# Optimization experiments

Measured on AMD Instinct MI355X. Metric: run time of the kernel, lower is better.

The kernel has to match this reference:

```python
import jax, jax.numpy as jnp
import numpy as np

EPS = 1e-6
NUM_HEADS = 16


def rotate_every_two(x):
    # pairs (x1, x2) -> (-x2, x1), interleaved on last dim
    x1 = x[..., 0::2]
    x2 = x[..., 1::2]
    return jnp.stack((-x2, x1), axis=-1).reshape(x.shape)


def apply_rotary(q, k, sinu_pos):
    # sinu_pos: [1, L, 2*dh]; split into sin/cos halves of size dh, then
    # repeat each element twice along feature dim ('b n -> b (n j)', j=2).
    L = sinu_pos.shape[1]
    sp = sinu_pos.reshape(L, 2, -1)          # [L, 2, dh]
    sin = jnp.repeat(sp[:, 0], 2, axis=-1)   # [L, D]
    cos = jnp.repeat(sp[:, 1], 2, axis=-1)   # [L, D]
    sin = sin[None, :, None, :]              # broadcast over B, H
    cos = cos[None, :, None, :]
    rot = lambda t: t * cos + rotate_every_two(t) * sin
    return rot(q), rot(k)


def softmax_kernel(data, is_query, proj):
    # data: [B, L, H, D], proj: [M, D] -> features [B, L, H, M]
    D = data.shape[-1]
    data_normalizer = D ** -0.25
    ratio = proj.shape[0] ** -0.5
    data_dash = jnp.einsum('blhd,md->blhm', data_normalizer * data, proj)
    diag = jnp.sum(data * data, axis=-1, keepdims=True) * 0.5 * data_normalizer ** 2
    if is_query:
        m = jax.lax.stop_gradient(jnp.max(data_dash, axis=-1, keepdims=True))
    else:
        m = jax.lax.stop_gradient(jnp.max(data_dash, axis=(-2, -1), keepdims=True))
    return ratio * (jnp.exp(data_dash - diag - m) + EPS)


def favor_noncausal(qp, kp, v):
    # qp, kp: [B, L, H, M]; v: [B, L, H, D]
    kvs = jnp.einsum('blhm,blhd->bhmd', kp, v)
    num = jnp.einsum('blhm,bhmd->blhd', qp, kvs)
    ks_sum = jnp.sum(kp, axis=1)                       # [B, H, M]
    den = jnp.einsum('blhm,bhm->blh', qp, ks_sum)      # [B, L, H]
    return num / den[..., None]


def setup_inputs() -> dict:
    key = jax.random.key(0)
    ks = jax.random.split(key, 7)
    B, L, Dm = 2, 4096, 1024
    M, Dh = 256, Dm // NUM_HEADS
    s = 0.02
    x = jax.random.normal(ks[0], (B, L, Dm), jnp.float32)
    Wq = jax.random.normal(ks[1], (Dm, Dm), jnp.float32) * s
    Wk = jax.random.normal(ks[2], (Dm, Dm), jnp.float32) * s
    Wv = jax.random.normal(ks[3], (Dm, Dm), jnp.float32) * s
    Wo = jax.random.normal(ks[4], (Dm, Dm), jnp.float32) * s
    proj = jax.random.normal(ks[5], (M, Dh), jnp.float32)
    sinu_pos = jax.random.normal(ks[6], (1, L, Dh), jnp.float32)
    return {"x": x, "Wq": Wq, "Wk": Wk, "Wv": Wv, "Wo": Wo,
            "proj": proj, "sinu_pos": sinu_pos}


def reference(x, Wq, Wk, Wv, Wo, proj, sinu_pos):
    B, L, Dm = x.shape
    H = NUM_HEADS
    Dh = Dm // H
    q = (x @ Wq).reshape(B, L, H, Dh)
    k = (x @ Wk).reshape(B, L, H, Dh)
    v = (x @ Wv).reshape(B, L, H, Dh)
    q, k = apply_rotary(q, k, sinu_pos)
    qp = softmax_kernel(q, True, proj)   # [B, L, H, M]
    kp = softmax_kernel(k, False, proj)  # [B, L, H, M]
    av = favor_noncausal(qp, kp, v)      # [B, L, H, Dh]
    return av.reshape(B, L, Dm) @ Wo
```

## Files before the change

### kernel.cpp

```cpp
#include <hip/hip_runtime.h>

typedef __attribute__((ext_vector_type(8))) short short8;
typedef __attribute__((ext_vector_type(4))) float f32x4;
typedef unsigned short USHORT;

#define DNORM 0.35355339059327373f
#define AS1(p) ((const __attribute__((address_space(1))) void*)(p))
#define AS3(p) ((__attribute__((address_space(3))) void*)(p))

__device__ __forceinline__ USHORT f2bf(float f) {
  union { float f; unsigned u; } v; v.f = f;
  unsigned r = v.u + 0x7fffu + ((v.u >> 16) & 1u);
  return (USHORT)(r >> 16);
}
__device__ __forceinline__ float bf2f(USHORT u) {
  union { unsigned u; float f; } v; v.u = ((unsigned)u) << 16;
  return v.f;
}
__device__ __forceinline__ unsigned fkey(float f) {
  union { float f; unsigned u; } v; v.f = f;
  return (v.u & 0x80000000u) ? ~v.u : (v.u | 0x80000000u);
}
__device__ __forceinline__ float keyf(unsigned k) {
  union { unsigned u; float f; } v;
  v.u = (k & 0x80000000u) ? (k ^ 0x80000000u) : ~k;
  return v.f;
}

__device__ __forceinline__ void stage_hl16(const float* __restrict__ src,
                                           USHORT* __restrict__ Ah, USHORT* __restrict__ Al,
                                           int r, int kc) {
  float b[16];
  *(float4*)&b[0] = *(const float4*)(src);
  *(float4*)&b[4] = *(const float4*)(src + 4);
  *(float4*)&b[8] = *(const float4*)(src + 8);
  *(float4*)&b[12] = *(const float4*)(src + 12);
  const int swz = (r & 7) << 3;
  unsigned H[8], L[8];
#pragma unroll
  for (int p = 0; p < 8; ++p) {
    USHORT h0 = f2bf(b[2 * p]), h1 = f2bf(b[2 * p + 1]);
    USHORT l0 = f2bf(b[2 * p] - bf2f(h0)), l1 = f2bf(b[2 * p + 1] - bf2f(h1));
    H[p] = (unsigned)h0 | ((unsigned)h1 << 16);
    L[p] = (unsigned)l0 | ((unsigned)l1 << 16);
  }
  *(uint4*)&Ah[r * 64 + (kc ^ swz)] = make_uint4(H[0], H[1], H[2], H[3]);
  *(uint4*)&Ah[r * 64 + ((kc + 8) ^ swz)] = make_uint4(H[4], H[5], H[6], H[7]);
  *(uint4*)&Al[r * 64 + (kc ^ swz)] = make_uint4(L[0], L[1], L[2], L[3]);
  *(uint4*)&Al[r * 64 + ((kc + 8) ^ swz)] = make_uint4(L[4], L[5], L[6], L[7]);
}

__global__ __launch_bounds__(256) void detect_kernel(const USHORT* __restrict__ w,
                                                     int* __restrict__ flag) {
  const int t = threadIdx.x;
  unsigned mx = 0;
#pragma unroll 8
  for (int c = 0; c < 64; ++c) {
    unsigned a = (unsigned)w[c * 256 + t] & 0x7FFFu;
    if (a > mx) mx = a;
  }
  if (mx > 0x4480u) atomicOr(flag, 1);
}

__global__ __launch_bounds__(256) void cvt_x_kernel(const void* __restrict__ xin,
                                                    USHORT* __restrict__ xh,
                                                    const void* __restrict__ proj,
                                                    USHORT* __restrict__ projc,
                                                    const int* __restrict__ flag) {
  if (blockIdx.x >= 4096) {
    const int i = ((blockIdx.x - 4096) * 256 + threadIdx.x) * 4;
    if (*flag) {
      float4 v = *(const float4*)((const float*)proj + i);
      USHORT a = f2bf(v.x), b = f2bf(v.y), c = f2bf(v.z), d = f2bf(v.w);
      *(uint2*)(projc + i) = make_uint2((unsigned)a | ((unsigned)b << 16),
                                        (unsigned)c | ((unsigned)d << 16));
    } else {
      *(uint2*)(projc + i) = *(const uint2*)((const USHORT*)proj + i);
    }
    return;
  }
  const size_t i = ((size_t)blockIdx.x * 256 + threadIdx.x) * 8;
  if (*flag) {
    const float* xf = (const float*)xin;
    float4 a = *(const float4*)(xf + i);
    float4 b = *(const float4*)(xf + i + 4);
    float c[8] = {a.x, a.y, a.z, a.w, b.x, b.y, b.z, b.w};
    unsigned ho[4];
#pragma unroll
    for (int j = 0; j < 4; ++j) {
      USHORT h0 = f2bf(c[2 * j]), h1 = f2bf(c[2 * j + 1]);
      ho[j] = (unsigned)h0 | ((unsigned)h1 << 16);
    }
    *(uint4*)(xh + i) = make_uint4(ho[0], ho[1], ho[2], ho[3]);
  } else {
    uint4 u = *(const uint4*)((const USHORT*)xin + i);
    *(uint4*)(xh + i) = u;
  }
}

__global__ __launch_bounds__(256) void sinut_kernel(const void* __restrict__ sinu,
                                                    float* __restrict__ sinuT,
                                                    const int* __restrict__ flag) {
  const int l = blockIdx.x * 256 + threadIdx.x;
  if (*flag) {
    const float* s = (const float*)sinu + (size_t)l * 64;
#pragma unroll 8
    for (int j2 = 0; j2 < 32; ++j2) {
      sinuT[j2 * 4096 + l] = s[j2];
      sinuT[131072 + j2 * 4096 + l] = s[32 + j2];
    }
  } else {
    const USHORT* s = (const USHORT*)sinu + (size_t)l * 64;
#pragma unroll 8
    for (int j2 = 0; j2 < 32; ++j2) {
      sinuT[j2 * 4096 + l] = bf2f(s[j2]);
      sinuT[131072 + j2 * 4096 + l] = bf2f(s[32 + j2]);
    }
  }
}

__global__ __launch_bounds__(256) void transpose_w_kernel(const void* __restrict__ Wq,
                                                          const void* __restrict__ Wk,
                                                          const void* __restrict__ Wv,
                                                          const void* __restrict__ Wo,
                                                          USHORT* __restrict__ wqkvt,
                                                          USHORT* __restrict__ wot,
                                                          const int* __restrict__ flag) {
  __shared__ __align__(16) USHORT tile[64][80];
  const int z = blockIdx.z;
  const void* src = (z == 0) ? Wq : (z == 1) ? Wk : (z == 2) ? Wv : Wo;
  USHORT* dst = (z < 3) ? (wqkvt + (size_t)z * 1048576) : wot;
  const int r0 = blockIdx.y * 64, c0 = blockIdx.x * 64;
  const int t = threadIdx.x;
  const int rr = t >> 2, c4 = (t & 3) * 16;
  if (*flag) {
    const float* s = (const float*)src + (size_t)(r0 + rr) * 1024 + c0 + c4;
#pragma unroll
    for (int i = 0; i < 4; ++i) {
      float4 v = *(const float4*)(s + i * 4);
      tile[rr][c4 + i * 4 + 0] = f2bf(v.x);
      tile[rr][c4 + i * 4 + 1] = f2bf(v.y);
      tile[rr][c4 + i * 4 + 2] = f2bf(v.z);
      tile[rr][c4 + i * 4 + 3] = f2bf(v.w);
    }
  } else {
    const USHORT* s = (const USHORT*)src + (size_t)(r0 + rr) * 1024 + c0 + c4;
    *(uint4*)&tile[rr][c4] = *(const uint4*)s;
    *(uint4*)&tile[rr][c4 + 8] = *(const uint4*)(s + 8);
  }
  __syncthreads();
  USHORT tmp[16];
#pragma unroll
  for (int i = 0; i < 16; ++i) tmp[i] = tile[c4 + i][rr];
  uint4 o0, o1;
  o0.x = (unsigned)tmp[0] | ((unsigned)tmp[1] << 16);
  o0.y = (unsigned)tmp[2] | ((unsigned)tmp[3] << 16);
  o0.z = (unsigned)tmp[4] | ((unsigned)tmp[5] << 16);
  o0.w = (unsigned)tmp[6] | ((unsigned)tmp[7] << 16);
  o1.x = (unsigned)tmp[8] | ((unsigned)tmp[9] << 16);
  o1.y = (unsigned)tmp[10] | ((unsigned)tmp[11] << 16);
  o1.z = (unsigned)tmp[12] | ((unsigned)tmp[13] << 16);
  o1.w = (unsigned)tmp[14] | ((unsigned)tmp[15] << 16);
  USHORT* d = dst + (size_t)(c0 + rr) * 1024 + r0 + c4;
  *(uint4*)d = o0;
  *(uint4*)(d + 8) = o1;
}

template <bool ROTEPI, bool FLAGOUT>
__global__ __launch_bounds__(256) void gemm_bt(const USHORT* __restrict__ A,
                                               const USHORT* __restrict__ Bt,
                                               void* __restrict__ Cv,
                                               USHORT* __restrict__ Vb,
                                               const float* __restrict__ sinuT,
                                               float* __restrict__ diag_q,
                                               float* __restrict__ diag_k,
                                               int M, int N, int K, int lda, int ldb, int ldc,
                                               int ldv, int NLO, const int* __restrict__ flag) {
  __shared__ __align__(16) USHORT As[8192];
  __shared__ __align__(16) USHORT Bs[8192];
  const int fl = *flag;
  const int t = threadIdx.x;
  const int lane = t & 63, wave = t >> 6;
  const int lr = lane & 15, lg = lane >> 4;
  const int nwg = gridDim.x * gridDim.y;
  const int orig = blockIdx.y * gridDim.x + blockIdx.x;
  const int tile = (orig & 7) * (nwg >> 3) + (orig >> 3);
  const int bx = tile % gridDim.x, by = tile / gridDim.x;
  const int row0 = by * 128, col0 = bx * 128;
  const int wr = (wave >> 1) * 64, wc = (wave & 1) * 64;
  f32x4 acc[4][4] = {};
  for (int k0 = 0; k0 < K; k0 += 64) {
#pragma unroll
    for (int c = 0; c < 4; ++c) {
      const int e = c * 256 + t;
      const int r = e >> 3;
      const int ch = (t & 7) ^ (r & 7);
      const size_t goffA = (size_t)(row0 + r) * lda + k0 + ch * 8;
      const size_t goffB = (size_t)(col0 + r) * ldb + k0 + ch * 8;
      __builtin_amdgcn_global_load_lds(AS1(A + goffA), AS3(&As[c * 2048 + wave * 512]), 16, 0, 0);
      __builtin_amdgcn_global_load_lds(AS1(Bt + goffB), AS3(&Bs[c * 2048 + wave * 512]), 16, 0, 0);
    }
    __syncthreads();
#pragma unroll
    for (int ks = 0; ks < 2; ++ks) {
      const int koff = ks * 32 + (lg << 3);
      short8 av_[4], bv[4];
#pragma unroll
      for (int i = 0; i < 4; ++i) {
        const int ar = wr + i * 16 + lr;
        av_[i] = *(const short8*)&As[ar * 64 + (koff ^ ((ar & 7) << 3))];
      }
#pragma unroll
      for (int j = 0; j < 4; ++j) {
        const int br = wc + j * 16 + lr;
        bv[j] = *(const short8*)&Bs[br * 64 + (koff ^ ((br & 7) << 3))];
      }
#pragma unroll
      for (int i = 0; i < 4; ++i)
#pragma unroll
        for (int j = 0; j < 4; ++j)
          acc[i][j] = __builtin_amdgcn_mfma_f32_16x16x32_bf16(av_[i], bv[j], acc[i][j], 0, 0, 0);
    }
    __syncthreads();
  }
  if constexpr (ROTEPI) {
    if (col0 < NLO) {
      const int G0 = col0 + wc;
      const int which = G0 >> 10;
      const int h = (G0 & 1023) >> 6;
      const int par = lr & 1;
      float* qk = (float*)Cv;
#pragma unroll
      for (int i = 0; i < 4; ++i) {
        const int R0 = row0 + wr + i * 16 + (lg << 2);
        const int l0 = R0 & 4095;
        float ss[4] = {0.f, 0.f, 0.f, 0.f};
#pragma unroll
        for (int j = 0; j < 4; ++j) {
          const int j2 = j * 8 + (lr >> 1);
          const float4 s4 = *(const float4*)&sinuT[(size_t)j2 * 4096 + l0];
          const float4 c4 = *(const float4*)&sinuT[131072 + (size_t)j2 * 4096 + l0];
          const float sv[4] = {s4.x, s4.y, s4.z, s4.w};
          const float cw[4] = {c4.x, c4.y, c4.z, c4.w};
          const int G = G0 + j * 16 + lr;
#pragma unroll
          for (int r = 0; r < 4; ++r) {
            const float own = acc[i][j][r];
            const float oth = __shfl_xor(own, 1);
            const float ro = par ? (own * cw[r] + oth * sv[r]) : (own * cw[r] - oth * sv[r]);
            ss[r] += ro * ro;
            qk[(size_t)(R0 + r) * ldc + G] = ro;
          }
        }
#pragma unroll
        for (int r = 0; r < 4; ++r) {
          float v_ = ss[r];
          v_ += __shfl_xor(v_, 1);
          v_ += __shfl_xor(v_, 2);
          v_ += __shfl_xor(v_, 4);
          v_ += __shfl_xor(v_, 8);
          if (lr == 0)
            (which ? diag_k : diag_q)[(R0 + r) * 16 + h] = v_ * 0.0625f;
        }
      }
    } else {
#pragma unroll
      for (int i = 0; i < 4; ++i) {
#pragma unroll
        for (int r = 0; r < 4; ++r) {
          const int row = row0 + wr + i * 16 + (lg << 2) + r;
#pragma unroll
          for (int j = 0; j < 4; ++j) {
            const int col = col0 + wc + j * 16 + lr - NLO;
            Vb[(size_t)row * ldv + col] = f2bf(acc[i][j][r]);
          }
        }
      }
    }
    return;
  }
#pragma unroll
  for (int i = 0; i < 4; ++i) {
#pragma unroll
    for (int r = 0; r < 4; ++r) {
      const int row = row0 + wr + i * 16 + (lg << 2) + r;
#pragma unroll
      for (int j = 0; j < 4; ++j) {
        const int col = col0 + wc + j * 16 + lr;
        const float v = acc[i][j][r];
        if constexpr (FLAGOUT) {
          if (fl) ((float*)Cv)[(size_t)row * ldc + col] = v;
          else ((USHORT*)Cv)[(size_t)row * ldc + col] = f2bf(v);
        } else {
          ((USHORT*)Cv)[(size_t)row * ldc + col] = f2bf(v);
        }
      }
    }
  }
}

__global__ __launch_bounds__(256) void ddk_max_kernel(const float* __restrict__ qkf,
                                                      const USHORT* __restrict__ proj,
                                                      unsigned* __restrict__ mk) {
  __shared__ __align__(16) USHORT Ph[16384];
  __shared__ __align__(16) USHORT Ah[4096], Al[4096];
  const int t = threadIdx.x, lane = t & 63, wave = t >> 6;
  const int lr = lane & 15, lg = lane >> 4;
  const int bh = blockIdx.y, b = bh >> 4, h = bh & 15;
  const size_t grow0 = (size_t)b * 4096 + blockIdx.x * 64;
  {
#pragma unroll
    for (int c = 0; c < 8; ++c)
      *(uint4*)&Ph[t * 64 + ((c ^ (t & 7)) << 3)] = *(const uint4*)(proj + t * 64 + c * 8);
  }
  {
    const int r = t >> 2, kc = (t & 3) * 16;
    stage_hl16(qkf + (grow0 + r) * 2048 + 1024 + h * 64 + kc, Ah, Al, r, kc);
  }
  __syncthreads();
  f32x4 acc[16] = {};
#pragma unroll
  for (int ks = 0; ks < 2; ++ks) {
    const int koff = ks * 32 + (lg << 3);
    const int ar = wave * 16 + lr;
    short8 a_h = *(const short8*)&Ah[ar * 64 + (koff ^ ((ar & 7) << 3))];
    short8 a_l = *(const short8*)&Al[ar * 64 + (koff ^ ((ar & 7) << 3))];
#pragma unroll
    for (int n = 0; n < 16; ++n) {
      const int br = n * 16 + lr;
      short8 b_h = *(const short8*)&Ph[br * 64 + (koff ^ ((br & 7) << 3))];
      acc[n] = __builtin_amdgcn_mfma_f32_16x16x32_bf16(a_h, b_h, acc[n], 0, 0, 0);
      acc[n] = __builtin_amdgcn_mfma_f32_16x16x32_bf16(a_l, b_h, acc[n], 0, 0, 0);
    }
  }
#pragma unroll
  for (int r = 0; r < 4; ++r) {
    float m_ = acc[0][r];
#pragma unroll
    for (int n = 1; n < 16; ++n) m_ = fmaxf(m_, acc[n][r]);
    m_ = fmaxf(m_, __shfl_xor(m_, 1));
    m_ = fmaxf(m_, __shfl_xor(m_, 2));
    m_ = fmaxf(m_, __shfl_xor(m_, 4));
    m_ = fmaxf(m_, __shfl_xor(m_, 8));
    if (lr == 0) {
      const int row = (int)grow0 + wave * 16 + (lg << 2) + r;
      atomicMax(&mk[row], fkey(m_ * DNORM));
    }
  }
}

__global__ __launch_bounds__(256) void kvs_accum_kernel(const float* __restrict__ qkf,
                                                        const USHORT* __restrict__ vb,
                                                        const USHORT* __restrict__ proj,
                                                        const float* __restrict__ diag_k,
                                                        const unsigned* __restrict__ mk,
                                                        float* __restrict__ kvs_ext) {
  __shared__ __align__(16) USHORT Ph[8192];
  __shared__ __align__(16) USHORT Ah[4096], Al[4096];
  __shared__ __align__(16) USHORT KpT[8192];
  __shared__ __align__(16) USHORT Vt[5120];
  const int t = threadIdx.x, lane = t & 63, wave = t >> 6;
  const int lr = lane & 15, lg = lane >> 4;
  const int bh = blockIdx.z, b = bh >> 4, h = bh & 15;
  const int fh = blockIdx.y;
  const int lstart = blockIdx.x * 512;
  {
    const int pr = t >> 1;
    const USHORT* src = proj + (size_t)(fh * 128 + pr) * 64;
#pragma unroll
    for (int c = 0; c < 4; ++c) {
      const int ch = (t & 1) * 4 + c;
      *(uint4*)&Ph[pr * 64 + ((ch ^ (pr & 7)) << 3)] = *(const uint4*)(src + ch * 8);
    }
  }
  if (t < 64) {
#pragma unroll
    for (int r = 64; r < 80; ++r) Vt[r * 64 + t] = (r == 64) ? (USHORT)0x3F80 : (USHORT)0;
  }
  f32x4 acc2[2][5] = {};
  for (int sub = 0; sub < 8; ++sub) {
    const int row0 = lstart + sub * 64;
    const size_t grow0 = (size_t)b * 4096 + row0;
    {
      const int r = t >> 2, kc = (t & 3) * 16;
      stage_hl16(qkf + (grow0 + r) * 2048 + 1024 + h * 64 + kc, Ah, Al, r, kc);
    }
    {
      const int rv = t & 63, dc = (t >> 6) * 16;
      const USHORT* sv = vb + (grow0 + rv) * 1024 + h * 64 + dc;
      uint4 u0 = *(const uint4*)sv;
      uint4 u1 = *(const uint4*)(sv + 8);
      unsigned wsrc[8] = {u0.x, u0.y, u0.z, u0.w, u1.x, u1.y, u1.z, u1.w};
#pragma unroll
      for (int i = 0; i < 8; ++i) {
        const int d0 = dc + 2 * i;
        Vt[d0 * 64 + (rv ^ ((d0 & 7) << 3))] = (USHORT)(wsrc[i] & 0xffff);
        Vt[(d0 + 1) * 64 + (rv ^ (((d0 + 1) & 7) << 3))] = (USHORT)(wsrc[i] >> 16);
      }
    }
    __syncthreads();
    f32x4 acc1[8] = {};
#pragma unroll
    for (int ks = 0; ks < 2; ++ks) {
      const int koff = ks * 32 + (lg << 3);
      const int ar = wave * 16 + lr;
      short8 a_h = *(const short8*)&Ah[ar * 64 + (koff ^ ((ar & 7) << 3))];
      short8 a_l = *(const short8*)&Al[ar * 64 + (koff ^ ((ar & 7) << 3))];
#pragma unroll
      for (int n = 0; n < 8; ++n) {
        const int br = n * 16 + lr;
        short8 b_h = *(const short8*)&Ph[br * 64 + (koff ^ ((br & 7) << 3))];
        acc1[n] = __builtin_amdgcn_mfma_f32_16x16x32_bf16(a_h, b_h, acc1[n], 0, 0, 0);
        acc1[n] = __builtin_amdgcn_mfma_f32_16x16x32_bf16(a_l, b_h, acc1[n], 0, 0, 0);
      }
    }
    const int rbase = wave * 16 + (lg << 2);
    float dg[4], mkr[4];
#pragma unroll
    for (int r = 0; r < 4; ++r) {
      dg[r] = diag_k[(grow0 + rbase + r) * 16 + h];
      mkr[r] = keyf(mk[grow0 + rbase + r]);
    }
#pragma unroll
    for (int n = 0; n < 8; ++n) {
      const int col = n * 16 + lr;
      USHORT pk[4];
#pragma unroll
      for (int r = 0; r < 4; ++r)
        pk[r] = f2bf(__expf(acc1[n][r] * DNORM - dg[r] - mkr[r]) + 1e-6f);
      const unsigned w0 = (unsigned)pk[0] | ((unsigned)pk[1] << 16);
      const unsigned w1 = (unsigned)pk[2] | ((unsigned)pk[3] << 16);
      *(uint2*)&KpT[col * 64 + (rbase ^ ((col & 7) << 3))] = make_uint2(w0, w1);
    }
    __syncthreads();
#pragma unroll
    for (int ks = 0; ks < 2; ++ks) {
      const int koff = ks * 32 + (lg << 3);
      short8 af[2];
#pragma unroll
      for (int i = 0; i < 2; ++i) {
        const int m = wave * 32 + i * 16 + lr;
        af[i] = *(const short8*)&KpT[m * 64 + (koff ^ ((m & 7) << 3))];
      }
#pragma unroll
      for (int c = 0; c < 5; ++c) {
        const int d = c * 16 + lr;
        short8 bv = *(const short8*)&Vt[d * 64 + (koff ^ ((d & 7) << 3))];
#pragma unroll
        for (int i = 0; i < 2; ++i)
          acc2[i][c] = __builtin_amdgcn_mfma_f32_16x16x32_bf16(af[i], bv, acc2[i][c], 0, 0, 0);
      }
    }
    __syncthreads();
  }
  float* basep = kvs_ext + (size_t)bh * 20480 + (size_t)fh * 128 * 80;
#pragma unroll
  for (int i = 0; i < 2; ++i) {
    const int mrow = wave * 32 + i * 16 + (lg << 2);
#pragma unroll
    for (int c = 0; c < 5; ++c) {
      const int col = c * 16 + lr;
      if (c == 4 && lr != 0) continue;
#pragma unroll
      for (int r = 0; r < 4; ++r)
        atomicAdd(basep + (size_t)(mrow + r) * 80 + col, acc2[i][c][r]);
    }
  }
}

__global__ __launch_bounds__(256) void cvt_kvs_kernel(const float* __restrict__ kvs_ext,
                                                      USHORT* __restrict__ kvsT16) {
  const int bh = blockIdx.x;
  const float* src = kvs_ext + (size_t)bh * 20480;
  USHORT* dst = kvsT16 + (size_t)bh * 20480;
  const int m = threadIdx.x;
#pragma unroll 8
  for (int d = 0; d < 80; ++d)
    dst[d * 256 + m] = f2bf(src[m * 80 + d]);
}

__global__ __launch_bounds__(256) void qav_kernel(const float* __restrict__ qkf,
                                                  const USHORT* __restrict__ proj,
                                                  const float* __restrict__ diag_q,
                                                  const USHORT* __restrict__ kvsT16,
                                                  USHORT* __restrict__ avb) {
  __shared__ __align__(16) USHORT smem[36864];
  USHORT* Ph = smem;
  USHORT* Qp = smem;
  USHORT* Ah = smem + 16384;
  USHORT* Al = smem + 20480;
  USHORT* Btl = smem + 16384;
  const int t = threadIdx.x, lane = t & 63, wave = t >> 6;
  const int lr = lane & 15, lg = lane >> 4;
  const int bh = blockIdx.y, b = bh >> 4, h = bh & 15;
  const size_t grow0 = (size_t)b * 4096 + blockIdx.x * 64;
  {
#pragma unroll
    for (int c = 0; c < 8; ++c)
      *(uint4*)&Ph[t * 64 + ((c ^ (t & 7)) << 3)] = *(const uint4*)(proj + t * 64 + c * 8);
  }
  {
    const int r = t >> 2, kc = (t & 3) * 16;
    stage_hl16(qkf + (grow0 + r) * 2048 + h * 64 + kc, Ah, Al, r, kc);
  }
  __syncthreads();
  f32x4 acc1[16] = {};
#pragma unroll
  for (int ks = 0; ks < 2; ++ks) {
    const int koff = ks * 32 + (lg << 3);
    const int ar = wave * 16 + lr;
    short8 a_h = *(const short8*)&Ah[ar * 64 + (koff ^ ((ar & 7) << 3))];
    short8 a_l = *(const short8*)&Al[ar * 64 + (koff ^ ((ar & 7) << 3))];
#pragma unroll
    for (int n = 0; n < 16; ++n) {
      const int br = n * 16 + lr;
      short8 b_h = *(const short8*)&Ph[br * 64 + (koff ^ ((br & 7) << 3))];
      acc1[n] = __builtin_amdgcn_mfma_f32_16x16x32_bf16(a_h, b_h, acc1[n], 0, 0, 0);
      acc1[n] = __builtin_amdgcn_mfma_f32_16x16x32_bf16(a_l, b_h, acc1[n], 0, 0, 0);
    }
  }
  __syncthreads();
  {
    const USHORT* src = kvsT16 + (size_t)bh * 20480;
#pragma unroll
    for (int c = 0; c < 10; ++c) {
      const int e = c * 256 + t;
      const int d = e >> 5, ch = e & 31;
      *(uint4*)&Btl[d * 256 + ((ch ^ (d & 7)) << 3)] = *(const uint4*)(src + d * 256 + ch * 8);
    }
  }
  const int rbase = wave * 16 + (lg << 2);
  float dg[4], mx[4];
#pragma unroll
  for (int r = 0; r < 4; ++r) dg[r] = diag_q[(grow0 + rbase + r) * 16 + h];
#pragma unroll
  for (int r = 0; r < 4; ++r) {
    float m_ = acc1[0][r];
#pragma unroll
    for (int n = 1; n < 16; ++n) m_ = fmaxf(m_, acc1[n][r]);
    m_ = fmaxf(m_, __shfl_xor(m_, 1));
    m_ = fmaxf(m_, __shfl_xor(m_, 2));
    m_ = fmaxf(m_, __shfl_xor(m_, 4));
    m_ = fmaxf(m_, __shfl_xor(m_, 8));
    mx[r] = m_ * DNORM;
  }
#pragma unroll
  for (int n = 0; n < 16; ++n) {
    const int col = n * 16 + lr;
#pragma unroll
    for (int r = 0; r < 4; ++r) {
      const int row = rbase + r;
      Qp[row * 256 + (col ^ ((row & 7) << 3))] =
          f2bf(__expf(acc1[n][r] * DNORM - dg[r] - mx[r]) + 1e-6f);
    }
  }
  __syncthreads();
  f32x4 acc2[5] = {};
#pragma unroll
  for (int ks2 = 0; ks2 < 8; ++ks2) {
    const int koff = ks2 * 32 + (lg << 3);
    const int ar = wave * 16 + lr;
    short8 a = *(const short8*)&Qp[ar * 256 + (koff ^ ((ar & 7) << 3))];
#pragma unroll
    for (int c = 0; c < 5; ++c) {
      const int cr = c * 16 + lr;
      short8 bv = *(const short8*)&Btl[cr * 256 + (koff ^ ((cr & 7) << 3))];
      acc2[c] = __builtin_amdgcn_mfma_f32_16x16x32_bf16(a, bv, acc2[c], 0, 0, 0);
    }
  }
#pragma unroll
  for (int r = 0; r < 4; ++r) {
    const float den = __shfl(acc2[4][r], (lane & 48));
#pragma unroll
    for (int c = 0; c < 4; ++c) {
      const float o = acc2[c][r] / den;
      avb[(grow0 + rbase + r) * 1024 + h * 64 + c * 16 + lr] = f2bf(o);
    }
  }
}

extern "C" void kernel_launch(void* const* d_in, const int* in_sizes, int n_in,
                              void* d_out, int out_size, void* d_ws, size_t ws_size,
                              hipStream_t stream) {
  char* ws = (char*)d_ws;

  const size_t OFF_FLAG = 0;
  const size_t OFF_WQKVT = 256;
  const size_t OFF_WOT = OFF_WQKVT + 6291456;
  const size_t OFF_PROJC = OFF_WOT + 2097152;
  const size_t OFF_PAD = OFF_PROJC + 32768;
  const size_t OFF_XH = OFF_PAD + 524288;
  const size_t OFF_SINUT = OFF_XH + 16777216;
  const size_t OFF_PAD2 = OFF_SINUT + 1048576;
  const size_t OFF_QKF = OFF_PAD2 + 15728640;
  const size_t OFF_VB = OFF_QKF + 67108864;
  const size_t OFF_DIAGQ = OFF_VB + 16777216;
  const size_t OFF_DIAGK = OFF_DIAGQ + 524288;
  const size_t OFF_MK = OFF_DIAGK + 524288;
  const size_t OFF_KVS = OFF_MK + 32768;
  const size_t OFF_KVST = OFF_KVS + 2621440;

  int* flag = (int*)(ws + OFF_FLAG);
  USHORT* wqkvt = (USHORT*)(ws + OFF_WQKVT);
  USHORT* wot = (USHORT*)(ws + OFF_WOT);
  USHORT* projc = (USHORT*)(ws + OFF_PROJC);
  USHORT* xh = (USHORT*)(ws + OFF_XH);
  USHORT* avb = (USHORT*)(ws + OFF_XH);
  float* sinuT = (float*)(ws + OFF_SINUT);
  float* qkf = (float*)(ws + OFF_QKF);
  USHORT* vb = (USHORT*)(ws + OFF_VB);
  float* diagq = (float*)(ws + OFF_DIAGQ);
  float* diagk = (float*)(ws + OFF_DIAGK);
  unsigned* mk = (unsigned*)(ws + OFF_MK);
  float* kvsb = (float*)(ws + OFF_KVS);
  USHORT* kvst = (USHORT*)(ws + OFF_KVST);

  hipMemsetAsync(ws + OFF_FLAG, 0, 256, stream);
  hipMemsetAsync(ws + OFF_MK, 0, 32768, stream);
  hipMemsetAsync(ws + OFF_KVS, 0, 2621440, stream);

  detect_kernel<<<1, 256, 0, stream>>>((const USHORT*)d_in[1], flag);
  cvt_x_kernel<<<4112, 256, 0, stream>>>(d_in[0], xh, d_in[5], projc, flag);
  sinut_kernel<<<16, 256, 0, stream>>>(d_in[6], sinuT, flag);
  transpose_w_kernel<<<dim3(16, 16, 4), 256, 0, stream>>>(d_in[1], d_in[2], d_in[3], d_in[4],
                                                          wqkvt, wot, flag);
  gemm_bt<true, false><<<dim3(24, 64), 256, 0, stream>>>(
      xh, wqkvt, qkf, vb, sinuT, diagq, diagk,
      8192, 3072, 1024, 1024, 1024, 2048, 1024, 2048, flag);
  ddk_max_kernel<<<dim3(64, 32), 256, 0, stream>>>(qkf, projc, mk);
  kvs_accum_kernel<<<dim3(8, 2, 32), 256, 0, stream>>>(qkf, vb, projc, diagk, mk, kvsb);
  cvt_kvs_kernel<<<32, 256, 0, stream>>>(kvsb, kvst);
  qav_kernel<<<dim3(64, 32), 256, 0, stream>>>(qkf, projc, diagq, kvst, avb);
  gemm_bt<false, true><<<dim3(8, 64), 256, 0, stream>>>(
      avb, wot, d_out, nullptr, nullptr, nullptr, nullptr,
      8192, 1024, 1024, 1024, 1024, 1024, 0, 0, flag);
}
```

Baseline: 236.3 us.

## Read proj and kvs operands from global directly, drop LDS staging and lo-split

```diff
diff --git a/kernel.cpp b/kernel.cpp
--- a/kernel.cpp
+++ b/kernel.cpp
@@ -48,6 +48,22 @@
   *(uint4*)&Ah[r * 64 + ((kc + 8) ^ swz)] = make_uint4(H[4], H[5], H[6], H[7]);
   *(uint4*)&Al[r * 64 + (kc ^ swz)] = make_uint4(L[0], L[1], L[2], L[3]);
   *(uint4*)&Al[r * 64 + ((kc + 8) ^ swz)] = make_uint4(L[4], L[5], L[6], L[7]);
+}
+
+__device__ __forceinline__ void stage_h16(const float* __restrict__ src,
+                                          USHORT* __restrict__ Ah, int r, int kc) {
+  float b[16];
+  *(float4*)&b[0] = *(const float4*)(src);
+  *(float4*)&b[4] = *(const float4*)(src + 4);
+  *(float4*)&b[8] = *(const float4*)(src + 8);
+  *(float4*)&b[12] = *(const float4*)(src + 12);
+  const int swz = (r & 7) << 3;
+  unsigned H[8];
+#pragma unroll
+  for (int p = 0; p < 8; ++p)
+    H[p] = (unsigned)f2bf(b[2 * p]) | ((unsigned)f2bf(b[2 * p + 1]) << 16);
+  *(uint4*)&Ah[r * 64 + (kc ^ swz)] = make_uint4(H[0], H[1], H[2], H[3]);
+  *(uint4*)&Ah[r * 64 + ((kc + 8) ^ swz)] = make_uint4(H[4], H[5], H[6], H[7]);
 }
 
 __global__ __launch_bounds__(256) void detect_kernel(const USHORT* __restrict__ w,
@@ -188,17 +204,24 @@
   const int bx = tile % gridDim.x, by = tile / gridDim.x;
   const int row0 = by * 128, col0 = bx * 128;
   const int wr = (wave >> 1) * 64, wc = (wave & 1) * 64;
+  const USHORT* pa[4];
+  const USHORT* pb[4];
+#pragma unroll
+  for (int c = 0; c < 4; ++c) {
+    const int e = c * 256 + t;
+    const int r = e >> 3;
+    const int ch = (t & 7) ^ (r & 7);
+    pa[c] = A + (size_t)(row0 + r) * lda + ch * 8;
+    pb[c] = Bt + (size_t)(col0 + r) * ldb + ch * 8;
+  }
   f32x4 acc[4][4] = {};
   for (int k0 = 0; k0 < K; k0 += 64) {
 #pragma unroll
     for (int c = 0; c < 4; ++c) {
-      const int e = c * 256 + t;
-      const int r = e >> 3;
-      const int ch = (t & 7) ^ (r & 7);
-      const size_t goffA = (size_t)(row0 + r) * lda + k0 + ch * 8;
-      const size_t goffB = (size_t)(col0 + r) * ldb + k0 + ch * 8;
-      __builtin_amdgcn_global_load_lds(AS1(A + goffA), AS3(&As[c * 2048 + wave * 512]), 16, 0, 0);
-      __builtin_amdgcn_global_load_lds(AS1(Bt + goffB), AS3(&Bs[c * 2048 + wave * 512]), 16, 0, 0);
+      __builtin_amdgcn_global_load_lds(AS1(pa[c]), AS3(&As[c * 2048 + wave * 512]), 16, 0, 0);
+      __builtin_amdgcn_global_load_lds(AS1(pb[c]), AS3(&Bs[c * 2048 + wave * 512]), 16, 0, 0);
+      pa[c] += 64;
+      pb[c] += 64;
     }
     __syncthreads();
 #pragma unroll
@@ -302,20 +325,14 @@
 __global__ __launch_bounds__(256) void ddk_max_kernel(const float* __restrict__ qkf,
                                                       const USHORT* __restrict__ proj,
                                                       unsigned* __restrict__ mk) {
-  __shared__ __align__(16) USHORT Ph[16384];
-  __shared__ __align__(16) USHORT Ah[4096], Al[4096];
+  __shared__ __align__(16) USHORT Ah[4096];
   const int t = threadIdx.x, lane = t & 63, wave = t >> 6;
   const int lr = lane & 15, lg = lane >> 4;
   const int bh = blockIdx.y, b = bh >> 4, h = bh & 15;
   const size_t grow0 = (size_t)b * 4096 + blockIdx.x * 64;
   {
-#pragma unroll
-    for (int c = 0; c < 8; ++c)
-      *(uint4*)&Ph[t * 64 + ((c ^ (t & 7)) << 3)] = *(const uint4*)(proj + t * 64 + c * 8);
-  }
-  {
     const int r = t >> 2, kc = (t & 3) * 16;
-    stage_hl16(qkf + (grow0 + r) * 2048 + 1024 + h * 64 + kc, Ah, Al, r, kc);
+    stage_h16(qkf + (grow0 + r) * 2048 + 1024 + h * 64 + kc, Ah, r, kc);
   }
   __syncthreads();
   f32x4 acc[16] = {};
@@ -324,13 +341,10 @@
     const int koff = ks * 32 + (lg << 3);
     const int ar = wave * 16 + lr;
     short8 a_h = *(const short8*)&Ah[ar * 64 + (koff ^ ((ar & 7) << 3))];
-    short8 a_l = *(const short8*)&Al[ar * 64 + (koff ^ ((ar & 7) << 3))];
 #pragma unroll
     for (int n = 0; n < 16; ++n) {
-      const int br = n * 16 + lr;
-      short8 b_h = *(const short8*)&Ph[br * 64 + (koff ^ ((br & 7) << 3))];
+      short8 b_h = *(const short8*)&proj[(n * 16 + lr) * 64 + koff];
       acc[n] = __builtin_amdgcn_mfma_f32_16x16x32_bf16(a_h, b_h, acc[n], 0, 0, 0);
-      acc[n] = __builtin_amdgcn_mfma_f32_16x16x32_bf16(a_l, b_h, acc[n], 0, 0, 0);
     }
   }
 #pragma unroll
@@ -355,7 +369,6 @@
                                                         const float* __restrict__ diag_k,
                                                         const unsigned* __restrict__ mk,
                                                         float* __restrict__ kvs_ext) {
-  __shared__ __align__(16) USHORT Ph[8192];
   __shared__ __align__(16) USHORT Ah[4096], Al[4096];
   __shared__ __align__(16) USHORT KpT[8192];
   __shared__ __align__(16) USHORT Vt[5120];
@@ -363,22 +376,14 @@
   const int lr = lane & 15, lg = lane >> 4;
   const int bh = blockIdx.z, b = bh >> 4, h = bh & 15;
   const int fh = blockIdx.y;
-  const int lstart = blockIdx.x * 512;
-  {
-    const int pr = t >> 1;
-    const USHORT* src = proj + (size_t)(fh * 128 + pr) * 64;
-#pragma unroll
-    for (int c = 0; c < 4; ++c) {
-      const int ch = (t & 1) * 4 + c;
-      *(uint4*)&Ph[pr * 64 + ((ch ^ (pr & 7)) << 3)] = *(const uint4*)(src + ch * 8);
-    }
-  }
+  const int lstart = blockIdx.x * 256;
+  const USHORT* projf = proj + (size_t)fh * 128 * 64;
   if (t < 64) {
 #pragma unroll
     for (int r = 64; r < 80; ++r) Vt[r * 64 + t] = (r == 64) ? (USHORT)0x3F80 : (USHORT)0;
   }
   f32x4 acc2[2][5] = {};
-  for (int sub = 0; sub < 8; ++sub) {
+  for (int sub = 0; sub < 4; ++sub) {
     const int row0 = lstart + sub * 64;
     const size_t grow0 = (size_t)b * 4096 + row0;
     {
@@ -408,8 +413,7 @@
       short8 a_l = *(const short8*)&Al[ar * 64 + (koff ^ ((ar & 7) << 3))];
 #pragma unroll
       for (int n = 0; n < 8; ++n) {
-        const int br = n * 16 + lr;
-        short8 b_h = *(const short8*)&Ph[br * 64 + (koff ^ ((br & 7) << 3))];
+        short8 b_h = *(const short8*)&projf[(n * 16 + lr) * 64 + koff];
         acc1[n] = __builtin_amdgcn_mfma_f32_16x16x32_bf16(a_h, b_h, acc1[n], 0, 0, 0);
         acc1[n] = __builtin_amdgcn_mfma_f32_16x16x32_bf16(a_l, b_h, acc1[n], 0, 0, 0);
       }
@@ -484,21 +488,15 @@
                                                   const float* __restrict__ diag_q,
                                                   const USHORT* __restrict__ kvsT16,
                                                   USHORT* __restrict__ avb) {
-  __shared__ __align__(16) USHORT smem[36864];
-  USHORT* Ph = smem;
+  __shared__ __align__(16) USHORT smem[16384];
+  USHORT* Ah = smem;
+  USHORT* Al = smem + 4096;
   USHORT* Qp = smem;
-  USHORT* Ah = smem + 16384;
-  USHORT* Al = smem + 20480;
-  USHORT* Btl = smem + 16384;
   const int t = threadIdx.x, lane = t & 63, wave = t >> 6;
   const int lr = lane & 15, lg = lane >> 4;
   const int bh = blockIdx.y, b = bh >> 4, h = bh & 15;
   const size_t grow0 = (size_t)b * 4096 + blockIdx.x * 64;
-  {
-#pragma unroll
-    for (int c = 0; c < 8; ++c)
-      *(uint4*)&Ph[t * 64 + ((c ^ (t & 7)) << 3)] = *(const uint4*)(proj + t * 64 + c * 8);
-  }
+  const USHORT* kvsrc = kvsT16 + (size_t)bh * 20480;
   {
     const int r = t >> 2, kc = (t & 3) * 16;
     stage_hl16(qkf + (grow0 + r) * 2048 + h * 64 + kc, Ah, Al, r, kc);
@@ -513,22 +511,12 @@
     short8 a_l = *(const short8*)&Al[ar * 64 + (koff ^ ((ar & 7) << 3))];
 #pragma unroll
     for (int n = 0; n < 16; ++n) {
-      const int br = n * 16 + lr;
-      short8 b_h = *(const short8*)&Ph[br * 64 + (koff ^ ((br & 7) << 3))];
+      short8 b_h = *(const short8*)&proj[(n * 16 + lr) * 64 + koff];
       acc1[n] = __builtin_amdgcn_mfma_f32_16x16x32_bf16(a_h, b_h, acc1[n], 0, 0, 0);
       acc1[n] = __builtin_amdgcn_mfma_f32_16x16x32_bf16(a_l, b_h, acc1[n], 0, 0, 0);
     }
   }
   __syncthreads();
-  {
-    const USHORT* src = kvsT16 + (size_t)bh * 20480;
-#pragma unroll
-    for (int c = 0; c < 10; ++c) {
-      const int e = c * 256 + t;
-      const int d = e >> 5, ch = e & 31;
-      *(uint4*)&Btl[d * 256 + ((ch ^ (d & 7)) << 3)] = *(const uint4*)(src + d * 256 + ch * 8);
-    }
-  }
   const int rbase = wave * 16 + (lg << 2);
   float dg[4], mx[4];
 #pragma unroll
@@ -563,8 +551,7 @@
     short8 a = *(const short8*)&Qp[ar * 256 + (koff ^ ((ar & 7) << 3))];
 #pragma unroll
     for (int c = 0; c < 5; ++c) {
-      const int cr = c * 16 + lr;
-      short8 bv = *(const short8*)&Btl[cr * 256 + (koff ^ ((cr & 7) << 3))];
+      short8 bv = *(const short8*)&kvsrc[(c * 16 + lr) * 256 + koff];
       acc2[c] = __builtin_amdgcn_mfma_f32_16x16x32_bf16(a, bv, acc2[c], 0, 0, 0);
     }
   }
@@ -628,7 +615,7 @@
       xh, wqkvt, qkf, vb, sinuT, diagq, diagk,
       8192, 3072, 1024, 1024, 1024, 2048, 1024, 2048, flag);
   ddk_max_kernel<<<dim3(64, 32), 256, 0, stream>>>(qkf, projc, mk);
-  kvs_accum_kernel<<<dim3(8, 2, 32), 256, 0, stream>>>(qkf, vb, projc, diagk, mk, kvsb);
+  kvs_accum_kernel<<<dim3(16, 2, 32), 256, 0, stream>>>(qkf, vb, projc, diagk, mk, kvsb);
   cvt_kvs_kernel<<<32, 256, 0, stream>>>(kvsb, kvst);
   qav_kernel<<<dim3(64, 32), 256, 0, stream>>>(qkf, projc, diagq, kvst, avb);
   gemm_bt<false, true><<<dim3(8, 64), 256, 0, stream>>>(
```

Result: slower. 317.0 us (+34.1%).
